# Performance work log

Measured on AMD Instinct MI355X. Metric: run time of the kernel, lower is better.

## Reference

```python
import jax, jax.numpy as jnp
import numpy as np

GRID = (32, 32)
LATENT = 256
ALPHA = 1.0
DECAY = 0.9


def _cdist(a, b):
    # Euclidean pairwise distance with a grad-safe sqrt (0 where d2==0, like torch.cdist).
    d2 = jnp.sum(a * a, -1)[:, None] + jnp.sum(b * b, -1)[None, :] - 2.0 * (a @ b.T)
    d2 = jnp.maximum(d2, 0.0)
    mask = d2 > 0
    return jnp.where(mask, jnp.sqrt(jnp.where(mask, d2, 1.0)), 0.0)


def setup_inputs() -> dict:
    key = jax.random.key(0)
    k1, k2 = jax.random.split(key)
    z = jax.random.normal(k1, (64, 512, 256), dtype=jnp.float32)
    nodes = jax.random.normal(k2, (GRID[0], GRID[1], LATENT), dtype=jnp.float32)
    return {"z": z, "nodes": nodes}


def reference(z, nodes):
    b, t, d = z.shape
    # time_decay^(seq_len - t - 1)
    tw = DECAY ** (t - 1 - jnp.arange(t, dtype=jnp.float32))
    z_flat = (z * tw[None, :, None]).reshape(b * t, d)   # (b t) d
    nodes_flat = nodes.reshape(-1, d)                     # n d

    dist = _cdist(z_flat, nodes_flat)                     # (b t) n
    q = 1.0 / (1.0 + dist / ALPHA) ** ((ALPHA + 1.0) / 2.0)
    q = q / jnp.sum(q, axis=-1, keepdims=True)            # L1 normalize rows
    q2 = q * q
    p = q2 / jnp.sum(q2, axis=0, keepdims=True)
    p = p / jnp.sum(p, axis=-1, keepdims=True)

    bmu = jnp.argmin(dist, axis=-1).reshape(b, t)         # int32

    # F.kl_div(q.log(), p, reduction='batchmean') = sum(p*(log p - log q)) / N
    kl_loss = jnp.sum(p * (jnp.log(p) - jnp.log(q))) / (b * t)
    diversity_loss = -jnp.mean(_cdist(nodes_flat, nodes_flat))
    time_smooth_loss = jnp.mean((z[:, 1:] - z[:, :-1]) ** 2) * DECAY

    # vectorized neighborhood consistency (python loop in the original is an
    # unweighted mean over all (b, t) adjacent pairs since seq_len is uniform)
    gw = GRID[1]
    pc = jnp.stack([bmu[:, :-1] // gw, bmu[:, :-1] % gw], axis=-1)
    nc = jnp.stack([bmu[:, 1:] // gw, bmu[:, 1:] % gw], axis=-1)
    neighbor_loss = jnp.mean(jnp.sum(jnp.abs(pc - nc), axis=-1).astype(jnp.float32))

    total_loss = kl_loss + 0.5 * diversity_loss + 0.3 * time_smooth_loss + 0.2 * neighbor_loss

    bmu_nodes = nodes_flat[bmu.reshape(-1)].reshape(b, t, d)
    som_z = z + 0.1 * (bmu_nodes - z)
    return (som_z, total_loss, kl_loss, diversity_loss, time_smooth_loss, neighbor_loss, q, bmu)
```

## Files before the change

### kernel.cpp

```cpp
#include <hip/hip_runtime.h>
#include <math.h>

#define Bb 64
#define Tt 512
#define Dd 256
#define Nn 1024
#define NROWS 32768

#define OUT_SOM 0L
#define OUT_SCAL 8388608L
#define OUT_Q 8388613L
#define OUT_BMU 41943045L

typedef __attribute__((ext_vector_type(8))) short bf16x8;
typedef __attribute__((ext_vector_type(4))) float f32x4;
typedef unsigned long long u64;
typedef unsigned short ushortT;

static __device__ __forceinline__ unsigned short f2bf(float x) {
  unsigned int u = __float_as_uint(x);
  unsigned int r = (u + 0x7fffu + ((u >> 16) & 1u)) >> 16;
  return (unsigned short)r;
}
static __device__ __forceinline__ float bf2f(unsigned short b) {
  return __uint_as_float(((unsigned int)b) << 16);
}

static __device__ __forceinline__ float block_reduce_sum(float v, float* sb) {
#pragma unroll
  for (int o = 32; o > 0; o >>= 1) v += __shfl_down(v, o, 64);
  const int lane = threadIdx.x & 63, w = threadIdx.x >> 6;
  if (lane == 0) sb[w] = v;
  __syncthreads();
  return (threadIdx.x == 0) ? (sb[0] + sb[1] + sb[2] + sb[3]) : 0.0f;
}

__global__ __launch_bounds__(256) void k_conv(
    const float* __restrict__ z, const float* __restrict__ nodes,
    ushortT* __restrict__ zhiF, ushortT* __restrict__ zloF, float* __restrict__ zn,
    ushortT* __restrict__ nhiF, ushortT* __restrict__ nloF, float* __restrict__ nnorm) {
  __shared__ float sm[32 * 260];
  const int tid = threadIdx.x;
  if (blockIdx.x < 1024) {
    const int rt = blockIdx.x;
    const long row0 = (long)rt * 32;
    const int r = tid >> 3, c8 = tid & 7;
    const long rowg = row0 + r;
    const int t = (int)(rowg & (Tt - 1));
    const float tw = powf(0.9f, (float)(Tt - 1 - t));
    float nrm = 0.f;
#pragma unroll
    for (int k = 0; k < 8; ++k) {
      const int c4 = c8 + k * 8;
      float4 v = ((const float4*)(z + rowg * Dd))[c4];
      v.x *= tw; v.y *= tw; v.z *= tw; v.w *= tw;
      *(float4*)&sm[r * 260 + c4 * 4] = v;
      nrm += v.x * v.x + v.y * v.y + v.z * v.z + v.w * v.w;
    }
    nrm += __shfl_xor(nrm, 1, 64);
    nrm += __shfl_xor(nrm, 2, 64);
    nrm += __shfl_xor(nrm, 4, 64);
    if (c8 == 0) zn[rowg] = nrm;
    __syncthreads();
    ushort4* oh = (ushort4*)(zhiF + (long)rt * 8192);
    ushort4* ol = (ushort4*)(zloF + (long)rt * 8192);
#pragma unroll
    for (int i = 0; i < 8; ++i) {
      const int o4 = tid + 256 * i;
      const int e4 = (o4 & 1) * 4;
      const int r16 = (o4 >> 1) & 15;
      const int k8 = (o4 >> 5) & 3;
      const int g = (o4 >> 7) & 1;
      const int ks = o4 >> 8;
      const float* p = &sm[(g * 16 + r16) * 260 + ks * 32 + k8 * 8 + e4];
      const float4 v = *(const float4*)p;
      ushort4 h, l;
      h.x = f2bf(v.x); l.x = f2bf(v.x - bf2f(h.x));
      h.y = f2bf(v.y); l.y = f2bf(v.y - bf2f(h.y));
      h.z = f2bf(v.z); l.z = f2bf(v.z - bf2f(h.z));
      h.w = f2bf(v.w); l.w = f2bf(v.w - bf2f(h.w));
      oh[o4] = h;
      ol[o4] = l;
    }
  } else {
    const int ct = blockIdx.x - 1024;
    const int jr = tid >> 4, cg = tid & 15;
    const long nrow = (long)(ct * 16 + jr);
    float nrm = 0.f;
#pragma unroll
    for (int k = 0; k < 4; ++k) {
      const int c4 = cg + k * 16;
      const float4 v = ((const float4*)(nodes + nrow * Dd))[c4];
      *(float4*)&sm[jr * 260 + c4 * 4] = v;
      nrm += v.x * v.x + v.y * v.y + v.z * v.z + v.w * v.w;
    }
    nrm += __shfl_xor(nrm, 1, 64);
    nrm += __shfl_xor(nrm, 2, 64);
    nrm += __shfl_xor(nrm, 4, 64);
    nrm += __shfl_xor(nrm, 8, 64);
    if (cg == 0) nnorm[nrow] = nrm;
    __syncthreads();
    ushort4* oh = (ushort4*)(nhiF + (long)ct * 4096);
    ushort4* ol = (ushort4*)(nloF + (long)ct * 4096);
#pragma unroll
    for (int i = 0; i < 4; ++i) {
      const int o4 = tid + 256 * i;
      const int e4 = (o4 & 1) * 4;
      const int c16 = (o4 >> 1) & 15;
      const int k8 = (o4 >> 5) & 3;
      const int ks = o4 >> 7;
      const float* p = &sm[c16 * 260 + ks * 32 + k8 * 8 + e4];
      const float4 v = *(const float4*)p;
      ushort4 h, l;
      h.x = f2bf(v.x); l.x = f2bf(v.x - bf2f(h.x));
      h.y = f2bf(v.y); l.y = f2bf(v.y - bf2f(h.y));
      h.z = f2bf(v.z); l.z = f2bf(v.z - bf2f(h.z));
      h.w = f2bf(v.w); l.w = f2bf(v.w - bf2f(h.w));
      oh[o4] = h;
      ol[o4] = l;
    }
  }
}

__global__ __launch_bounds__(1024, 4) void k_gemm4(
    const ushortT* __restrict__ zhiF, const ushortT* __restrict__ zloF,
    const ushortT* __restrict__ nhiF, const ushortT* __restrict__ nloF,
    const float* __restrict__ zn, const float* __restrict__ nn,
    float* __restrict__ qout, float* __restrict__ bmuf, float* __restrict__ colsum) {
  __shared__ float srowS[32][16];
  __shared__ u64 sbmu[32][16];
  __shared__ float sinv[32];
  const int tid = threadIdx.x, lane = tid & 63, w = tid >> 6;
  const int rl = lane & 15, kq = lane >> 4;
  const int rt = blockIdx.x;
  const long row0 = (long)rt * 32;

  const ushortT* Ah = zhiF + (long)rt * 8192;
  const ushortT* Al = zloF + (long)rt * 8192;
  const ushortT* Bh = nhiF + (long)w * 4 * 4096;
  const ushortT* Bl = nloF + (long)w * 4 * 4096;
  const int lo8 = lane * 8;

  f32x4 acc[2][4];
#pragma unroll
  for (int g = 0; g < 2; ++g)
#pragma unroll
    for (int c = 0; c < 4; ++c) acc[g][c] = (f32x4){0.f, 0.f, 0.f, 0.f};

#pragma unroll 2
  for (int ks = 0; ks < 8; ++ks) {
    bf16x8 ah[2], al[2], bh[4], bl[4];
#pragma unroll
    for (int g = 0; g < 2; ++g) {
      ah[g] = *(const bf16x8*)(Ah + (ks * 2 + g) * 512 + lo8);
      al[g] = *(const bf16x8*)(Al + (ks * 2 + g) * 512 + lo8);
    }
#pragma unroll
    for (int c = 0; c < 4; ++c) {
      bh[c] = *(const bf16x8*)(Bh + c * 4096 + ks * 512 + lo8);
      bl[c] = *(const bf16x8*)(Bl + c * 4096 + ks * 512 + lo8);
    }
    __builtin_amdgcn_s_setprio(1);
#pragma unroll
    for (int c = 0; c < 4; ++c)
#pragma unroll
      for (int g = 0; g < 2; ++g) {
        acc[g][c] = __builtin_amdgcn_mfma_f32_16x16x32_bf16(ah[g], bh[c], acc[g][c], 0, 0, 0);
        acc[g][c] = __builtin_amdgcn_mfma_f32_16x16x32_bf16(ah[g], bl[c], acc[g][c], 0, 0, 0);
        acc[g][c] = __builtin_amdgcn_mfma_f32_16x16x32_bf16(al[g], bh[c], acc[g][c], 0, 0, 0);
      }
    __builtin_amdgcn_s_setprio(0);
  }

  float nnv[4];
#pragma unroll
  for (int c = 0; c < 4; ++c) nnv[c] = nn[w * 64 + c * 16 + rl];

  float rs[2][4];
  u64 bm[2][4];
#pragma unroll
  for (int g = 0; g < 2; ++g)
#pragma unroll
    for (int r = 0; r < 4; ++r) {
      rs[g][r] = 0.f;
      bm[g][r] = ~0ull;
    }
#pragma unroll
  for (int g = 0; g < 2; ++g) {
    float znv[4];
#pragma unroll
    for (int r = 0; r < 4; ++r) znv[r] = zn[row0 + g * 16 + kq * 4 + r];
#pragma unroll
    for (int c = 0; c < 4; ++c)
#pragma unroll
      for (int r = 0; r < 4; ++r) {
        const float dot = acc[g][c][r];
        const float d2 = znv[r] + nnv[c] - 2.f * dot;
        const float dist = sqrtf(fmaxf(d2, 0.f));
        const float qv = 1.f / (1.f + dist);
        acc[g][c][r] = qv;
        rs[g][r] += qv;
        const int col = w * 64 + c * 16 + rl;
        const u64 pk = ((u64)__float_as_uint(dist) << 32) | (unsigned int)col;
        bm[g][r] = pk < bm[g][r] ? pk : bm[g][r];
      }
  }
#pragma unroll
  for (int g = 0; g < 2; ++g)
#pragma unroll
    for (int r = 0; r < 4; ++r) {
#pragma unroll
      for (int m = 1; m < 16; m <<= 1) {
        rs[g][r] += __shfl_xor(rs[g][r], m, 64);
        const u64 o = __shfl_xor(bm[g][r], m, 64);
        bm[g][r] = o < bm[g][r] ? o : bm[g][r];
      }
      if (rl == 0) {
        srowS[g * 16 + kq * 4 + r][w] = rs[g][r];
        sbmu[g * 16 + kq * 4 + r][w] = bm[g][r];
      }
    }
  __syncthreads();
  if (tid < 32) {
    float s = 0.f;
    u64 best = ~0ull;
#pragma unroll
    for (int i = 0; i < 16; ++i) {
      s += srowS[tid][i];
      const u64 v = sbmu[tid][i];
      best = v < best ? v : best;
    }
    sinv[tid] = 1.f / s;
    bmuf[row0 + tid] = (float)(int)(unsigned int)(best & 0xffffffffull);
  }
  __syncthreads();

  float cp[4];
#pragma unroll
  for (int c = 0; c < 4; ++c) cp[c] = 0.f;
#pragma unroll
  for (int g = 0; g < 2; ++g) {
    float inv[4];
#pragma unroll
    for (int r = 0; r < 4; ++r) inv[r] = sinv[g * 16 + kq * 4 + r];
#pragma unroll
    for (int c = 0; c < 4; ++c)
#pragma unroll
      for (int r = 0; r < 4; ++r) {
        const float qn = acc[g][c][r] * inv[r];
        qout[(row0 + g * 16 + kq * 4 + r) * Nn + w * 64 + c * 16 + rl] = qn;
        cp[c] = fmaf(qn, qn, cp[c]);
      }
  }
#pragma unroll
  for (int c = 0; c < 4; ++c) {
    cp[c] += __shfl_xor(cp[c], 16, 64);
    cp[c] += __shfl_xor(cp[c], 32, 64);
    if (kq == 0) atomicAdd(&colsum[w * 64 + c * 16 + rl], cp[c]);
  }
}

__global__ __launch_bounds__(256) void k_div2(
    const ushortT* __restrict__ nhiF, const ushortT* __restrict__ nloF,
    const float* __restrict__ nnorm, float* __restrict__ scal) {
  __shared__ float sb[4];
  const int tid = threadIdx.x, lane = tid & 63, w = tid >> 6;
  const int rl = lane & 15, kq = lane >> 4;
  const int bi = blockIdx.x & 63;
  const int cq = blockIdx.x >> 6;
  const int lo8 = lane * 8;

  f32x4 acc[4];
#pragma unroll
  for (int c = 0; c < 4; ++c) acc[c] = (f32x4){0.f, 0.f, 0.f, 0.f};

#pragma unroll 2
  for (int ks = 0; ks < 8; ++ks) {
    const bf16x8 ah = *(const bf16x8*)(nhiF + (long)bi * 4096 + ks * 512 + lo8);
    const bf16x8 al = *(const bf16x8*)(nloF + (long)bi * 4096 + ks * 512 + lo8);
#pragma unroll
    for (int c = 0; c < 4; ++c) {
      const long ct = (long)(cq * 16 + w * 4 + c);
      const bf16x8 bh = *(const bf16x8*)(nhiF + ct * 4096 + ks * 512 + lo8);
      const bf16x8 bl = *(const bf16x8*)(nloF + ct * 4096 + ks * 512 + lo8);
      acc[c] = __builtin_amdgcn_mfma_f32_16x16x32_bf16(ah, bh, acc[c], 0, 0, 0);
      acc[c] = __builtin_amdgcn_mfma_f32_16x16x32_bf16(ah, bl, acc[c], 0, 0, 0);
      acc[c] = __builtin_amdgcn_mfma_f32_16x16x32_bf16(al, bh, acc[c], 0, 0, 0);
    }
  }
  float ni[4];
#pragma unroll
  for (int r = 0; r < 4; ++r) ni[r] = nnorm[bi * 16 + kq * 4 + r];
  float dsum = 0.f;
#pragma unroll
  for (int c = 0; c < 4; ++c) {
    const float nj = nnorm[(cq * 16 + w * 4 + c) * 16 + rl];
#pragma unroll
    for (int r = 0; r < 4; ++r) {
      const float d2 = ni[r] + nj - 2.f * acc[c][r];
      dsum += sqrtf(fmaxf(d2, 0.f));
    }
  }
  const float tot = block_reduce_sum(dsum, sb);
  if (tid == 0) atomicAdd(&scal[1], tot);
}

__global__ __launch_bounds__(256) void k_kl(const float* __restrict__ q,
                                            const float* __restrict__ colsum,
                                            float* __restrict__ scal) {
  __shared__ float4 rcs4[Nn / 4];
  __shared__ float4 lcs4[Nn / 4];
  __shared__ float sb[4];
  const int tid = threadIdx.x, lane = tid & 63, wave = tid >> 6;
  {
    const float c0 = colsum[tid * 4 + 0];
    const float c1 = colsum[tid * 4 + 1];
    const float c2 = colsum[tid * 4 + 2];
    const float c3 = colsum[tid * 4 + 3];
    rcs4[tid] = make_float4(1.f / c0, 1.f / c1, 1.f / c2, 1.f / c3);
    lcs4[tid] = make_float4(__logf(c0), __logf(c1), __logf(c2), __logf(c3));
  }
  __syncthreads();
  const long r0 = (long)blockIdx.x * 16;
  float klp = 0.f;
  for (int rr = 0; rr < 4; ++rr) {
    const long row = r0 + rr * 4 + wave;
    float s = 0.f, a = 0.f;
#pragma unroll
    for (int j = 0; j < 4; ++j) {
      const int c4 = lane + 64 * j;
      const float4 qv = *(const float4*)(q + row * Nn + c4 * 4);
      const float4 rc = rcs4[c4];
      const float4 lc = lcs4[c4];
      float u;
      u = qv.x * qv.x * rc.x; s += u; a = fmaf(u, __logf(qv.x) - lc.x, a);
      u = qv.y * qv.y * rc.y; s += u; a = fmaf(u, __logf(qv.y) - lc.y, a);
      u = qv.z * qv.z * rc.z; s += u; a = fmaf(u, __logf(qv.z) - lc.z, a);
      u = qv.w * qv.w * rc.w; s += u; a = fmaf(u, __logf(qv.w) - lc.w, a);
    }
#pragma unroll
    for (int o = 1; o < 64; o <<= 1) {
      s += __shfl_xor(s, o, 64);
      a += __shfl_xor(a, o, 64);
    }
    if (lane == 0) klp += a / s - __logf(s);
  }
  const float tot = block_reduce_sum(klp, sb);
  if (tid == 0) atomicAdd(&scal[0], tot);
}

__global__ __launch_bounds__(256) void k_somnb(const float* __restrict__ z,
                                               const float* __restrict__ nodes,
                                               const float* __restrict__ bmuf,
                                               float* __restrict__ som,
                                               float* __restrict__ scal) {
  __shared__ float sb[4];
  const int tid = threadIdx.x;
  const long r0 = (long)blockIdx.x * 16;
  float ts = 0.f, zp = 0.f;
  if ((r0 & (Tt - 1)) > 0) zp = z[(r0 - 1) * Dd + tid];
  for (int r = 0; r < 16; ++r) {
    const long row = r0 + r;
    const float zc = z[row * Dd + tid];
    const int bi = (int)bmuf[row];
    const float nv = nodes[(long)bi * Dd + tid];
    som[row * Dd + tid] = zc + 0.1f * (nv - zc);
    if ((row & (Tt - 1)) > 0) {
      const float dd = zc - zp;
      ts = fmaf(dd, dd, ts);
    }
    zp = zc;
  }
  const float tts = block_reduce_sum(ts, sb);
  if (tid == 0) atomicAdd(&scal[2], tts);
  float nbv = 0.f;
  if (tid < 16) {
    const long row = r0 + tid;
    if ((row & (Tt - 1)) != (Tt - 1)) {
      const int b1 = (int)bmuf[row], b2 = (int)bmuf[row + 1];
      nbv = (float)(abs((b1 >> 5) - (b2 >> 5)) + abs((b1 & 31) - (b2 & 31)));
    }
  }
  __syncthreads();
  const float tnb = block_reduce_sum(nbv, sb);
  if (tid == 0) atomicAdd(&scal[3], tnb);
}

__global__ void k_final(const float* __restrict__ scal, float* __restrict__ o) {
  const float kl = scal[0] * (1.f / 32768.f);
  const float dv = -scal[1] * (1.f / (1024.f * 1024.f));
  const float ts = scal[2] * (0.9f / (64.f * 511.f * 256.f));
  const float nb = scal[3] * (1.f / 32704.f);
  o[0] = kl + 0.5f * dv + 0.3f * ts + 0.2f * nb;
  o[1] = kl;
  o[2] = dv;
  o[3] = ts;
  o[4] = nb;
}

__global__ __launch_bounds__(256) void k_prep_fb(const float* __restrict__ nodes,
                                                 float* __restrict__ nt,
                                                 float* __restrict__ nnorm) {
  __shared__ float sb[4];
  const int j = blockIdx.x, d = threadIdx.x;
  const float v = nodes[j * Dd + d];
  nt[(long)d * Nn + j] = v;
  const float tot = block_reduce_sum(v * v, sb);
  if (threadIdx.x == 0) nnorm[j] = tot;
}

__global__ __launch_bounds__(256) void k_div_fb(const float* __restrict__ nodes,
                                                const float* __restrict__ nt,
                                                const float* __restrict__ nnorm,
                                                float* __restrict__ scal) {
  __shared__ float ni[4][Dd];
  __shared__ float sb[4];
  const int tid = threadIdx.x;
  const int i0 = blockIdx.x * 4;
#pragma unroll
  for (int r = 0; r < 4; ++r) ni[r][tid] = nodes[(i0 + r) * Dd + tid];
  __syncthreads();
  float acc[4][4];
#pragma unroll
  for (int r = 0; r < 4; ++r)
#pragma unroll
    for (int jj = 0; jj < 4; ++jj) acc[r][jj] = 0.f;
  for (int d = 0; d < Dd; ++d) {
    float nj[4];
#pragma unroll
    for (int jj = 0; jj < 4; ++jj) nj[jj] = nt[(long)d * Nn + tid + 256 * jj];
#pragma unroll
    for (int r = 0; r < 4; ++r) {
      const float s = ni[r][d];
#pragma unroll
      for (int jj = 0; jj < 4; ++jj) acc[r][jj] = fmaf(s, nj[jj], acc[r][jj]);
    }
  }
  float sum = 0.f;
#pragma unroll
  for (int r = 0; r < 4; ++r)
#pragma unroll
    for (int jj = 0; jj < 4; ++jj) {
      const float d2 = nnorm[i0 + r] + nnorm[tid + 256 * jj] - 2.f * acc[r][jj];
      sum += sqrtf(fmaxf(d2, 0.f));
    }
  const float tot = block_reduce_sum(sum, sb);
  if (tid == 0) atomicAdd(&scal[1], tot);
}

__global__ __launch_bounds__(256) void k_dist_fb(
    const float* __restrict__ z, const float* __restrict__ nt,
    const float* __restrict__ nnorm, float* __restrict__ qout,
    float* __restrict__ srow, float* __restrict__ bmuf) {
  __shared__ float zt[Dd][65];
  __shared__ float rs4[4][64];
  __shared__ u64 cand[4][64];
  const int tid = threadIdx.x, lane = tid & 63, wave = tid >> 6;
  const long row0 = (long)blockIdx.x * 64;
  for (int k = 0; k < 64; ++k) {
    const int t = (int)((row0 + k) & (Tt - 1));
    const float tw = powf(0.9f, (float)(Tt - 1 - t));
    zt[tid][k] = z[(row0 + k) * Dd + tid] * tw;
  }
  __syncthreads();
  float zns = 0.f;
  for (int d = 0; d < Dd; ++d) {
    const float v = zt[d][lane];
    zns = fmaf(v, v, zns);
  }
  const long myrow = row0 + lane;
  float rsum = 0.f;
  u64 best = ~0ull;
  const int j0w = wave * 256;
  for (int chunk = 0; chunk < 16; ++chunk) {
    const int j0 = j0w + chunk * 16;
    float acc[16];
#pragma unroll
    for (int i = 0; i < 16; ++i) acc[i] = 0.f;
    const float* ntp = nt + j0;
    for (int d = 0; d < Dd; ++d) {
      const float zv = zt[d][lane];
      const float4 a = ((const float4*)ntp)[0];
      const float4 b = ((const float4*)ntp)[1];
      const float4 c = ((const float4*)ntp)[2];
      const float4 e = ((const float4*)ntp)[3];
      ntp += Nn;
      acc[0] = fmaf(zv, a.x, acc[0]); acc[1] = fmaf(zv, a.y, acc[1]);
      acc[2] = fmaf(zv, a.z, acc[2]); acc[3] = fmaf(zv, a.w, acc[3]);
      acc[4] = fmaf(zv, b.x, acc[4]); acc[5] = fmaf(zv, b.y, acc[5]);
      acc[6] = fmaf(zv, b.z, acc[6]); acc[7] = fmaf(zv, b.w, acc[7]);
      acc[8] = fmaf(zv, c.x, acc[8]); acc[9] = fmaf(zv, c.y, acc[9]);
      acc[10] = fmaf(zv, c.z, acc[10]); acc[11] = fmaf(zv, c.w, acc[11]);
      acc[12] = fmaf(zv, e.x, acc[12]); acc[13] = fmaf(zv, e.y, acc[13]);
      acc[14] = fmaf(zv, e.z, acc[14]); acc[15] = fmaf(zv, e.w, acc[15]);
    }
#pragma unroll
    for (int jj = 0; jj < 16; ++jj) {
      const int j = j0 + jj;
      const float d2 = zns + nnorm[j] - 2.f * acc[jj];
      const float dist = sqrtf(fmaxf(d2, 0.f));
      const float qr = 1.f / (1.f + dist);
      qout[myrow * Nn + j] = qr;
      rsum += qr;
      const u64 pk = ((u64)__float_as_uint(dist) << 32) | (unsigned int)j;
      best = pk < best ? pk : best;
    }
  }
  rs4[wave][lane] = rsum;
  cand[wave][lane] = best;
  __syncthreads();
  if (wave == 0) {
    const float s = rs4[0][lane] + rs4[1][lane] + rs4[2][lane] + rs4[3][lane];
    srow[myrow] = s;
    const u64 m0 = cand[0][lane] < cand[1][lane] ? cand[0][lane] : cand[1][lane];
    const u64 m1 = cand[2][lane] < cand[3][lane] ? cand[2][lane] : cand[3][lane];
    const u64 m = m0 < m1 ? m0 : m1;
    bmuf[myrow] = (float)(int)(unsigned int)(m & 0xffffffffull);
  }
}

__global__ __launch_bounds__(256) void k_norm_fb(float* __restrict__ q,
                                                 const float* __restrict__ srow,
                                                 float* __restrict__ colsum) {
  const int tid = threadIdx.x;
  const long r0 = (long)blockIdx.x * 16;
  float cs[4] = {0.f, 0.f, 0.f, 0.f};
  for (int r = 0; r < 16; ++r) {
    const long row = r0 + r;
    const float inv = 1.f / srow[row];
#pragma unroll
    for (int j = 0; j < 4; ++j) {
      const long idx = row * Nn + tid + 256 * j;
      const float v = q[idx] * inv;
      q[idx] = v;
      cs[j] = fmaf(v, v, cs[j]);
    }
  }
#pragma unroll
  for (int j = 0; j < 4; ++j) atomicAdd(&colsum[tid + 256 * j], cs[j]);
}

extern "C" void kernel_launch(void* const* d_in, const int* in_sizes, int n_in,
                              void* d_out, int out_size, void* d_ws, size_t ws_size,
                              hipStream_t stream) {
  const float* z = (const float*)d_in[0];
  const float* nodes = (const float*)d_in[1];
  float* out = (float*)d_out;
  unsigned char* ws = (unsigned char*)d_ws;

  float* som = out + OUT_SOM;
  float* scal_out = out + OUT_SCAL;
  float* qout = out + OUT_Q;
  float* bmuf = out + OUT_BMU;

  const size_t NEED = 34742288;
  if (ws_size >= NEED) {
    ushortT* zhiF = (ushortT*)(ws + 0);
    ushortT* zloF = (ushortT*)(ws + 16777216);
    ushortT* nhiF = (ushortT*)(ws + 33554432);
    ushortT* nloF = (ushortT*)(ws + 34078720);
    float* zn = (float*)(ws + 34603008);
    float* nnorm = (float*)(ws + 34734080);
    float* colsum = (float*)(ws + 34738176);
    float* scal = (float*)(ws + 34742272);

    hipMemsetAsync(colsum, 0, 4096 + 16, stream);

    k_conv<<<1088, 256, 0, stream>>>(z, nodes, zhiF, zloF, zn, nhiF, nloF, nnorm);
    k_gemm4<<<1024, 1024, 0, stream>>>(zhiF, zloF, nhiF, nloF, zn, nnorm, qout, bmuf, colsum);
    k_div2<<<256, 256, 0, stream>>>(nhiF, nloF, nnorm, scal);
    k_kl<<<2048, 256, 0, stream>>>(qout, colsum, scal);
    k_somnb<<<2048, 256, 0, stream>>>(z, nodes, bmuf, som, scal);
    k_final<<<1, 1, 0, stream>>>(scal, scal_out);
  } else {
    float* wsf = (float*)ws;
    float* nt = wsf;
    float* nnorm = wsf + 262144;
    float* srow = wsf + 263168;
    float* colsum = wsf + 295936;
    float* scal = wsf + 296960;

    hipMemsetAsync(colsum, 0, (1024 + 4) * sizeof(float), stream);
    k_prep_fb<<<1024, 256, 0, stream>>>(nodes, nt, nnorm);
    k_div_fb<<<256, 256, 0, stream>>>(nodes, nt, nnorm, scal);
    k_dist_fb<<<512, 256, 0, stream>>>(z, nt, nnorm, qout, srow, bmuf);
    k_norm_fb<<<2048, 256, 0, stream>>>(qout, srow, colsum);
    k_kl<<<2048, 256, 0, stream>>>(qout, colsum, scal);
    k_somnb<<<2048, 256, 0, stream>>>(z, nodes, bmuf, som, scal);
    k_final<<<1, 1, 0, stream>>>(scal, scal_out);
  }
}
```

Before: 251.6 us.

## Restructure SOM pipeline: row-major split A, LDS-staged 64-row GEMM, fused tail kernel

The conversion kernel now writes z's hi/lo bf16 split in a simple row-major layout, one wave per row. The GEMM handles 64 rows per block and stages A into LDS with global_load_lds and an XOR swizzle. It runs the three split-precision MFMA passes as 24 sequential k-steps. Column sums are written as per-block partials and reduced by a new small kernel, which replaces the global atomics and the memset. The KL, SOM/neighbour and diversity kernels are merged into one launch; the trade-off is a larger workspace, a scalar KL loop, and more LDS per GEMM block, which may limit occupancy.

```diff
diff --git a/kernel.cpp b/kernel.cpp
--- a/kernel.cpp
+++ b/kernel.cpp
@@ -35,55 +35,32 @@
   return (threadIdx.x == 0) ? (sb[0] + sb[1] + sb[2] + sb[3]) : 0.0f;
 }
 
-__global__ __launch_bounds__(256) void k_conv(
+__global__ __launch_bounds__(256) void k_conv3(
     const float* __restrict__ z, const float* __restrict__ nodes,
-    ushortT* __restrict__ zhiF, ushortT* __restrict__ zloF, float* __restrict__ zn,
-    ushortT* __restrict__ nhiF, ushortT* __restrict__ nloF, float* __restrict__ nnorm) {
+    ushortT* __restrict__ A2, ushortT* __restrict__ nhiF, ushortT* __restrict__ nloF,
+    float* __restrict__ zn, float* __restrict__ nnorm) {
   __shared__ float sm[32 * 260];
   const int tid = threadIdx.x;
-  if (blockIdx.x < 1024) {
-    const int rt = blockIdx.x;
-    const long row0 = (long)rt * 32;
-    const int r = tid >> 3, c8 = tid & 7;
-    const long rowg = row0 + r;
-    const int t = (int)(rowg & (Tt - 1));
+  if (blockIdx.x < 8192) {
+    const int lane = tid & 63, w = tid >> 6;
+    const long row = (long)blockIdx.x * 4 + w;
+    const int t = (int)(row & (Tt - 1));
     const float tw = powf(0.9f, (float)(Tt - 1 - t));
-    float nrm = 0.f;
-#pragma unroll
-    for (int k = 0; k < 8; ++k) {
-      const int c4 = c8 + k * 8;
-      float4 v = ((const float4*)(z + rowg * Dd))[c4];
-      v.x *= tw; v.y *= tw; v.z *= tw; v.w *= tw;
-      *(float4*)&sm[r * 260 + c4 * 4] = v;
-      nrm += v.x * v.x + v.y * v.y + v.z * v.z + v.w * v.w;
-    }
-    nrm += __shfl_xor(nrm, 1, 64);
-    nrm += __shfl_xor(nrm, 2, 64);
-    nrm += __shfl_xor(nrm, 4, 64);
-    if (c8 == 0) zn[rowg] = nrm;
-    __syncthreads();
-    ushort4* oh = (ushort4*)(zhiF + (long)rt * 8192);
-    ushort4* ol = (ushort4*)(zloF + (long)rt * 8192);
-#pragma unroll
-    for (int i = 0; i < 8; ++i) {
-      const int o4 = tid + 256 * i;
-      const int e4 = (o4 & 1) * 4;
-      const int r16 = (o4 >> 1) & 15;
-      const int k8 = (o4 >> 5) & 3;
-      const int g = (o4 >> 7) & 1;
-      const int ks = o4 >> 8;
-      const float* p = &sm[(g * 16 + r16) * 260 + ks * 32 + k8 * 8 + e4];
-      const float4 v = *(const float4*)p;
-      ushort4 h, l;
-      h.x = f2bf(v.x); l.x = f2bf(v.x - bf2f(h.x));
-      h.y = f2bf(v.y); l.y = f2bf(v.y - bf2f(h.y));
-      h.z = f2bf(v.z); l.z = f2bf(v.z - bf2f(h.z));
-      h.w = f2bf(v.w); l.w = f2bf(v.w - bf2f(h.w));
-      oh[o4] = h;
-      ol[o4] = l;
-    }
+    const float4 v = ((const float4*)(z + row * Dd))[lane];
+    float x0 = v.x * tw, x1 = v.y * tw, x2 = v.z * tw, x3 = v.w * tw;
+    ushort4 h, l;
+    h.x = f2bf(x0); l.x = f2bf(x0 - bf2f(h.x));
+    h.y = f2bf(x1); l.y = f2bf(x1 - bf2f(h.y));
+    h.z = f2bf(x2); l.z = f2bf(x2 - bf2f(h.z));
+    h.w = f2bf(x3); l.w = f2bf(x3 - bf2f(h.w));
+    *(ushort4*)(A2 + row * 512 + lane * 4) = h;
+    *(ushort4*)(A2 + row * 512 + 256 + lane * 4) = l;
+    float s = x0 * x0 + x1 * x1 + x2 * x2 + x3 * x3;
+#pragma unroll
+    for (int o = 32; o > 0; o >>= 1) s += __shfl_down(s, o, 64);
+    if (lane == 0) zn[row] = s;
   } else {
-    const int ct = blockIdx.x - 1024;
+    const int ct = blockIdx.x - 8192;
     const int jr = tid >> 4, cg = tid & 15;
     const long nrow = (long)(ct * 16 + jr);
     float nrm = 0.f;
@@ -122,71 +99,77 @@
   }
 }
 
-__global__ __launch_bounds__(1024, 4) void k_gemm4(
-    const ushortT* __restrict__ zhiF, const ushortT* __restrict__ zloF,
-    const ushortT* __restrict__ nhiF, const ushortT* __restrict__ nloF,
-    const float* __restrict__ zn, const float* __restrict__ nn,
-    float* __restrict__ qout, float* __restrict__ bmuf, float* __restrict__ colsum) {
-  __shared__ float srowS[32][16];
-  __shared__ u64 sbmu[32][16];
-  __shared__ float sinv[32];
+__global__ __launch_bounds__(1024) void k_gemmF(
+    const ushortT* __restrict__ A2, const ushortT* __restrict__ nhiF,
+    const ushortT* __restrict__ nloF, const float* __restrict__ zn,
+    const float* __restrict__ nnorm, float* __restrict__ qout,
+    float* __restrict__ bmuf, float* __restrict__ psum) {
+  __shared__ __align__(16) unsigned char sA[65536];
+  __shared__ float srowS[64][16];
+  __shared__ u64 sbmu[64][16];
+  __shared__ float sinv[64];
   const int tid = threadIdx.x, lane = tid & 63, w = tid >> 6;
   const int rl = lane & 15, kq = lane >> 4;
-  const int rt = blockIdx.x;
-  const long row0 = (long)rt * 32;
-
-  const ushortT* Ah = zhiF + (long)rt * 8192;
-  const ushortT* Al = zloF + (long)rt * 8192;
-  const ushortT* Bh = nhiF + (long)w * 4 * 4096;
-  const ushortT* Bl = nloF + (long)w * 4 * 4096;
-  const int lo8 = lane * 8;
-
-  f32x4 acc[2][4];
-#pragma unroll
-  for (int g = 0; g < 2; ++g)
+  const long row0 = (long)blockIdx.x * 64;
+
+#pragma unroll
+  for (int i = 0; i < 4; ++i) {
+    const int flat = i * 1024 + tid;
+    const int r = flat >> 6, slot = flat & 63;
+    const int srcs = slot ^ (r & 7);
+    __builtin_amdgcn_global_load_lds(
+        (const __attribute__((address_space(1))) void*)(A2 + (row0 + r) * 512 + srcs * 8),
+        (__attribute__((address_space(3))) void*)(sA + flat * 16), 16, 0, 0);
+  }
+
+  const ushortT* Bh = nhiF + (long)(w * 4) * 4096 + lane * 8;
+  const ushortT* Bl = nloF + (long)(w * 4) * 4096 + lane * 8;
+
+  f32x4 acc[4][4];
+#pragma unroll
+  for (int g = 0; g < 4; ++g)
 #pragma unroll
     for (int c = 0; c < 4; ++c) acc[g][c] = (f32x4){0.f, 0.f, 0.f, 0.f};
 
-#pragma unroll 2
-  for (int ks = 0; ks < 8; ++ks) {
-    bf16x8 ah[2], al[2], bh[4], bl[4];
-#pragma unroll
-    for (int g = 0; g < 2; ++g) {
-      ah[g] = *(const bf16x8*)(Ah + (ks * 2 + g) * 512 + lo8);
-      al[g] = *(const bf16x8*)(Al + (ks * 2 + g) * 512 + lo8);
-    }
-#pragma unroll
-    for (int c = 0; c < 4; ++c) {
-      bh[c] = *(const bf16x8*)(Bh + c * 4096 + ks * 512 + lo8);
-      bl[c] = *(const bf16x8*)(Bl + c * 4096 + ks * 512 + lo8);
+  __syncthreads();
+
+#pragma unroll
+  for (int m = 0; m < 24; ++m) {
+    const int t3 = m >> 3, ks = m & 7;
+    const int abase = (t3 == 2) ? 32 : 0;
+    const ushortT* Bp = (t3 == 1) ? Bl : Bh;
+    bf16x8 b[4];
+#pragma unroll
+    for (int c = 0; c < 4; ++c) b[c] = *(const bf16x8*)(Bp + c * 4096 + ks * 512);
+    bf16x8 a[4];
+#pragma unroll
+    for (int g = 0; g < 4; ++g) {
+      const int rr = g * 16 + rl;
+      const int kslot = abase + ks * 4 + kq;
+      a[g] = *(const bf16x8*)(sA + rr * 1024 + ((kslot ^ (rr & 7)) << 4));
     }
     __builtin_amdgcn_s_setprio(1);
 #pragma unroll
-    for (int c = 0; c < 4; ++c)
-#pragma unroll
-      for (int g = 0; g < 2; ++g) {
-        acc[g][c] = __builtin_amdgcn_mfma_f32_16x16x32_bf16(ah[g], bh[c], acc[g][c], 0, 0, 0);
-        acc[g][c] = __builtin_amdgcn_mfma_f32_16x16x32_bf16(ah[g], bl[c], acc[g][c], 0, 0, 0);
-        acc[g][c] = __builtin_amdgcn_mfma_f32_16x16x32_bf16(al[g], bh[c], acc[g][c], 0, 0, 0);
-      }
+    for (int g = 0; g < 4; ++g)
+#pragma unroll
+      for (int c = 0; c < 4; ++c)
+        acc[g][c] = __builtin_amdgcn_mfma_f32_16x16x32_bf16(a[g], b[c], acc[g][c], 0, 0, 0);
     __builtin_amdgcn_s_setprio(0);
   }
 
   float nnv[4];
 #pragma unroll
-  for (int c = 0; c < 4; ++c) nnv[c] = nn[w * 64 + c * 16 + rl];
-
-  float rs[2][4];
-  u64 bm[2][4];
-#pragma unroll
-  for (int g = 0; g < 2; ++g)
-#pragma unroll
-    for (int r = 0; r < 4; ++r) {
-      rs[g][r] = 0.f;
-      bm[g][r] = ~0ull;
-    }
-#pragma unroll
-  for (int g = 0; g < 2; ++g) {
+  for (int c = 0; c < 4; ++c) nnv[c] = nnorm[w * 64 + c * 16 + rl];
+
+  float rs[4][4];
+  u64 bm[4][4];
+#pragma unroll
+  for (int g = 0; g < 4; ++g)
+#pragma unroll
+    for (int r = 0; r < 4; ++r) { rs[g][r] = 0.f; bm[g][r] = ~0ull; }
+
+#pragma unroll
+  for (int g = 0; g < 4; ++g) {
     float znv[4];
 #pragma unroll
     for (int r = 0; r < 4; ++r) znv[r] = zn[row0 + g * 16 + kq * 4 + r];
@@ -206,7 +189,7 @@
       }
   }
 #pragma unroll
-  for (int g = 0; g < 2; ++g)
+  for (int g = 0; g < 4; ++g)
 #pragma unroll
     for (int r = 0; r < 4; ++r) {
 #pragma unroll
@@ -221,7 +204,7 @@
       }
     }
   __syncthreads();
-  if (tid < 32) {
+  if (tid < 64) {
     float s = 0.f;
     u64 best = ~0ull;
 #pragma unroll
@@ -239,7 +222,7 @@
 #pragma unroll
   for (int c = 0; c < 4; ++c) cp[c] = 0.f;
 #pragma unroll
-  for (int g = 0; g < 2; ++g) {
+  for (int g = 0; g < 4; ++g) {
     float inv[4];
 #pragma unroll
     for (int r = 0; r < 4; ++r) inv[r] = sinv[g * 16 + kq * 4 + r];
@@ -256,134 +239,135 @@
   for (int c = 0; c < 4; ++c) {
     cp[c] += __shfl_xor(cp[c], 16, 64);
     cp[c] += __shfl_xor(cp[c], 32, 64);
-    if (kq == 0) atomicAdd(&colsum[w * 64 + c * 16 + rl], cp[c]);
-  }
-}
-
-__global__ __launch_bounds__(256) void k_div2(
-    const ushortT* __restrict__ nhiF, const ushortT* __restrict__ nloF,
-    const float* __restrict__ nnorm, float* __restrict__ scal) {
-  __shared__ float sb[4];
-  const int tid = threadIdx.x, lane = tid & 63, w = tid >> 6;
-  const int rl = lane & 15, kq = lane >> 4;
-  const int bi = blockIdx.x & 63;
-  const int cq = blockIdx.x >> 6;
-  const int lo8 = lane * 8;
-
-  f32x4 acc[4];
-#pragma unroll
-  for (int c = 0; c < 4; ++c) acc[c] = (f32x4){0.f, 0.f, 0.f, 0.f};
-
+    if (kq == 0) psum[(long)blockIdx.x * Nn + w * 64 + c * 16 + rl] = cp[c];
+  }
+}
+
+__global__ __launch_bounds__(256) void k_cs(const float* __restrict__ psum,
+                                            float* __restrict__ colsum) {
+  __shared__ float sh[4][64];
+  const int c = threadIdx.x & 63, sl = threadIdx.x >> 6;
+  const int col = blockIdx.x * 64 + c;
+  float s = 0.f;
+#pragma unroll 4
+  for (int p = sl * 128; p < sl * 128 + 128; ++p) s += psum[(long)p * Nn + col];
+  sh[sl][c] = s;
+  __syncthreads();
+  if (sl == 0) colsum[col] = sh[0][c] + sh[1][c] + sh[2][c] + sh[3][c];
+}
+
+__global__ __launch_bounds__(256) void k_tail(
+    const float* __restrict__ q, const float* __restrict__ colsum,
+    const float* __restrict__ z, const float* __restrict__ nodes,
+    const float* __restrict__ bmuf, const ushortT* __restrict__ nhiF,
+    const ushortT* __restrict__ nloF, const float* __restrict__ nnorm,
+    float* __restrict__ som, float* __restrict__ scal) {
+  __shared__ float sh[2052];
+  const int tid = threadIdx.x, lane = tid & 63, wave = tid >> 6;
+  const int bid = blockIdx.x;
+  if (bid < 2048) {
+    float* rcs = sh;
+    float* lcs = sh + 1024;
+    float* sb = sh + 2048;
+#pragma unroll
+    for (int j = 0; j < 4; ++j) {
+      const float cs = colsum[tid + 256 * j];
+      rcs[tid + 256 * j] = 1.f / cs;
+      lcs[tid + 256 * j] = __logf(cs);
+    }
+    __syncthreads();
+    const long r0 = (long)bid * 16;
+    float klp = 0.f;
+    for (int rr = 0; rr < 4; ++rr) {
+      const long row = r0 + rr * 4 + wave;
+      float s = 0.f, a = 0.f;
+#pragma unroll
+      for (int j = 0; j < 16; ++j) {
+        const int col = lane + 64 * j;
+        const float t = q[row * Nn + col];
+        const float u = t * t * rcs[col];
+        s += u;
+        a = fmaf(u, __logf(t) - lcs[col], a);
+      }
+#pragma unroll
+      for (int o = 1; o < 64; o <<= 1) {
+        s += __shfl_xor(s, o, 64);
+        a += __shfl_xor(a, o, 64);
+      }
+      if (lane == 0) klp += a / s - __logf(s);
+    }
+    const float tot = block_reduce_sum(klp, sb);
+    if (tid == 0) atomicAdd(&scal[0], tot);
+  } else if (bid < 4096) {
+    float* sb = sh;
+    const long r0 = (long)(bid - 2048) * 16;
+    float ts = 0.f, zp = 0.f;
+    if ((r0 & (Tt - 1)) > 0) zp = z[(r0 - 1) * Dd + tid];
+    for (int r = 0; r < 16; ++r) {
+      const long row = r0 + r;
+      const float zc = z[row * Dd + tid];
+      const int bi = (int)bmuf[row];
+      const float nv = nodes[(long)bi * Dd + tid];
+      som[row * Dd + tid] = zc + 0.1f * (nv - zc);
+      if ((row & (Tt - 1)) > 0) {
+        const float dd = zc - zp;
+        ts = fmaf(dd, dd, ts);
+      }
+      zp = zc;
+    }
+    const float tts = block_reduce_sum(ts, sb);
+    if (tid == 0) atomicAdd(&scal[2], tts);
+    float nbv = 0.f;
+    if (tid < 16) {
+      const long row = r0 + tid;
+      if ((row & (Tt - 1)) != (Tt - 1)) {
+        const int b1 = (int)bmuf[row], b2 = (int)bmuf[row + 1];
+        nbv = (float)(abs((b1 >> 5) - (b2 >> 5)) + abs((b1 & 31) - (b2 & 31)));
+      }
+    }
+    __syncthreads();
+    const float tnb = block_reduce_sum(nbv, sb);
+    if (tid == 0) atomicAdd(&scal[3], tnb);
+  } else {
+    float* sb = sh;
+    const int w = wave;
+    const int rl = lane & 15, kq = lane >> 4;
+    const int bi = (bid - 4096) & 63;
+    const int cq = (bid - 4096) >> 6;
+    const int lo8 = lane * 8;
+    f32x4 acc[4];
+#pragma unroll
+    for (int c = 0; c < 4; ++c) acc[c] = (f32x4){0.f, 0.f, 0.f, 0.f};
 #pragma unroll 2
-  for (int ks = 0; ks < 8; ++ks) {
-    const bf16x8 ah = *(const bf16x8*)(nhiF + (long)bi * 4096 + ks * 512 + lo8);
-    const bf16x8 al = *(const bf16x8*)(nloF + (long)bi * 4096 + ks * 512 + lo8);
+    for (int ks = 0; ks < 8; ++ks) {
+      const bf16x8 ah = *(const bf16x8*)(nhiF + (long)bi * 4096 + ks * 512 + lo8);
+      const bf16x8 al = *(const bf16x8*)(nloF + (long)bi * 4096 + ks * 512 + lo8);
+#pragma unroll
+      for (int c = 0; c < 4; ++c) {
+        const long ct = (long)(cq * 16 + w * 4 + c);
+        const bf16x8 bh = *(const bf16x8*)(nhiF + ct * 4096 + ks * 512 + lo8);
+        const bf16x8 bl = *(const bf16x8*)(nloF + ct * 4096 + ks * 512 + lo8);
+        acc[c] = __builtin_amdgcn_mfma_f32_16x16x32_bf16(ah, bh, acc[c], 0, 0, 0);
+        acc[c] = __builtin_amdgcn_mfma_f32_16x16x32_bf16(ah, bl, acc[c], 0, 0, 0);
+        acc[c] = __builtin_amdgcn_mfma_f32_16x16x32_bf16(al, bh, acc[c], 0, 0, 0);
+      }
+    }
+    float ni[4];
+#pragma unroll
+    for (int r = 0; r < 4; ++r) ni[r] = nnorm[bi * 16 + kq * 4 + r];
+    float dsum = 0.f;
 #pragma unroll
     for (int c = 0; c < 4; ++c) {
-      const long ct = (long)(cq * 16 + w * 4 + c);
-      const bf16x8 bh = *(const bf16x8*)(nhiF + ct * 4096 + ks * 512 + lo8);
-      const bf16x8 bl = *(const bf16x8*)(nloF + ct * 4096 + ks * 512 + lo8);
-      acc[c] = __builtin_amdgcn_mfma_f32_16x16x32_bf16(ah, bh, acc[c], 0, 0, 0);
-      acc[c] = __builtin_amdgcn_mfma_f32_16x16x32_bf16(ah, bl, acc[c], 0, 0, 0);
-      acc[c] = __builtin_amdgcn_mfma_f32_16x16x32_bf16(al, bh, acc[c], 0, 0, 0);
-    }
-  }
-  float ni[4];
-#pragma unroll
-  for (int r = 0; r < 4; ++r) ni[r] = nnorm[bi * 16 + kq * 4 + r];
-  float dsum = 0.f;
-#pragma unroll
-  for (int c = 0; c < 4; ++c) {
-    const float nj = nnorm[(cq * 16 + w * 4 + c) * 16 + rl];
-#pragma unroll
-    for (int r = 0; r < 4; ++r) {
-      const float d2 = ni[r] + nj - 2.f * acc[c][r];
-      dsum += sqrtf(fmaxf(d2, 0.f));
-    }
-  }
-  const float tot = block_reduce_sum(dsum, sb);
-  if (tid == 0) atomicAdd(&scal[1], tot);
-}
-
-__global__ __launch_bounds__(256) void k_kl(const float* __restrict__ q,
-                                            const float* __restrict__ colsum,
-                                            float* __restrict__ scal) {
-  __shared__ float4 rcs4[Nn / 4];
-  __shared__ float4 lcs4[Nn / 4];
-  __shared__ float sb[4];
-  const int tid = threadIdx.x, lane = tid & 63, wave = tid >> 6;
-  {
-    const float c0 = colsum[tid * 4 + 0];
-    const float c1 = colsum[tid * 4 + 1];
-    const float c2 = colsum[tid * 4 + 2];
-    const float c3 = colsum[tid * 4 + 3];
-    rcs4[tid] = make_float4(1.f / c0, 1.f / c1, 1.f / c2, 1.f / c3);
-    lcs4[tid] = make_float4(__logf(c0), __logf(c1), __logf(c2), __logf(c3));
-  }
-  __syncthreads();
-  const long r0 = (long)blockIdx.x * 16;
-  float klp = 0.f;
-  for (int rr = 0; rr < 4; ++rr) {
-    const long row = r0 + rr * 4 + wave;
-    float s = 0.f, a = 0.f;
-#pragma unroll
-    for (int j = 0; j < 4; ++j) {
-      const int c4 = lane + 64 * j;
-      const float4 qv = *(const float4*)(q + row * Nn + c4 * 4);
-      const float4 rc = rcs4[c4];
-      const float4 lc = lcs4[c4];
-      float u;
-      u = qv.x * qv.x * rc.x; s += u; a = fmaf(u, __logf(qv.x) - lc.x, a);
-      u = qv.y * qv.y * rc.y; s += u; a = fmaf(u, __logf(qv.y) - lc.y, a);
-      u = qv.z * qv.z * rc.z; s += u; a = fmaf(u, __logf(qv.z) - lc.z, a);
-      u = qv.w * qv.w * rc.w; s += u; a = fmaf(u, __logf(qv.w) - lc.w, a);
-    }
-#pragma unroll
-    for (int o = 1; o < 64; o <<= 1) {
-      s += __shfl_xor(s, o, 64);
-      a += __shfl_xor(a, o, 64);
-    }
-    if (lane == 0) klp += a / s - __logf(s);
-  }
-  const float tot = block_reduce_sum(klp, sb);
-  if (tid == 0) atomicAdd(&scal[0], tot);
-}
-
-__global__ __launch_bounds__(256) void k_somnb(const float* __restrict__ z,
-                                               const float* __restrict__ nodes,
-                                               const float* __restrict__ bmuf,
-                                               float* __restrict__ som,
-                                               float* __restrict__ scal) {
-  __shared__ float sb[4];
-  const int tid = threadIdx.x;
-  const long r0 = (long)blockIdx.x * 16;
-  float ts = 0.f, zp = 0.f;
-  if ((r0 & (Tt - 1)) > 0) zp = z[(r0 - 1) * Dd + tid];
-  for (int r = 0; r < 16; ++r) {
-    const long row = r0 + r;
-    const float zc = z[row * Dd + tid];
-    const int bi = (int)bmuf[row];
-    const float nv = nodes[(long)bi * Dd + tid];
-    som[row * Dd + tid] = zc + 0.1f * (nv - zc);
-    if ((row & (Tt - 1)) > 0) {
-      const float dd = zc - zp;
-      ts = fmaf(dd, dd, ts);
-    }
-    zp = zc;
-  }
-  const float tts = block_reduce_sum(ts, sb);
-  if (tid == 0) atomicAdd(&scal[2], tts);
-  float nbv = 0.f;
-  if (tid < 16) {
-    const long row = r0 + tid;
-    if ((row & (Tt - 1)) != (Tt - 1)) {
-      const int b1 = (int)bmuf[row], b2 = (int)bmuf[row + 1];
-      nbv = (float)(abs((b1 >> 5) - (b2 >> 5)) + abs((b1 & 31) - (b2 & 31)));
-    }
-  }
-  __syncthreads();
-  const float tnb = block_reduce_sum(nbv, sb);
-  if (tid == 0) atomicAdd(&scal[3], tnb);
+      const float nj = nnorm[(cq * 16 + w * 4 + c) * 16 + rl];
+#pragma unroll
+      for (int r = 0; r < 4; ++r) {
+        const float d2 = ni[r] + nj - 2.f * acc[c][r];
+        dsum += sqrtf(fmaxf(d2, 0.f));
+      }
+    }
+    const float tot = block_reduce_sum(dsum, sb);
+    if (tid == 0) atomicAdd(&scal[1], tot);
+  }
 }
 
 __global__ void k_final(const float* __restrict__ scal, float* __restrict__ o) {
@@ -540,6 +524,81 @@
   for (int j = 0; j < 4; ++j) atomicAdd(&colsum[tid + 256 * j], cs[j]);
 }
 
+__global__ __launch_bounds__(256) void k_kl_fb(const float* __restrict__ q,
+                                               const float* __restrict__ colsum,
+                                               float* __restrict__ scal) {
+  __shared__ float rcs[Nn];
+  __shared__ float lcs[Nn];
+  __shared__ float sb[4];
+  const int tid = threadIdx.x, lane = tid & 63, wave = tid >> 6;
+#pragma unroll
+  for (int j = 0; j < 4; ++j) {
+    const float cs = colsum[tid + 256 * j];
+    rcs[tid + 256 * j] = 1.f / cs;
+    lcs[tid + 256 * j] = __logf(cs);
+  }
+  __syncthreads();
+  const long r0 = (long)blockIdx.x * 16;
+  float klp = 0.f;
+  for (int rr = 0; rr < 4; ++rr) {
+    const long row = r0 + rr * 4 + wave;
+    float s = 0.f, a = 0.f;
+#pragma unroll
+    for (int j = 0; j < 16; ++j) {
+      const int col = lane + 64 * j;
+      const float t = q[row * Nn + col];
+      const float u = t * t * rcs[col];
+      s += u;
+      a = fmaf(u, __logf(t) - lcs[col], a);
+    }
+#pragma unroll
+    for (int o = 1; o < 64; o <<= 1) {
+      s += __shfl_xor(s, o, 64);
+      a += __shfl_xor(a, o, 64);
+    }
+    if (lane == 0) klp += a / s - __logf(s);
+  }
+  const float tot = block_reduce_sum(klp, sb);
+  if (tid == 0) atomicAdd(&scal[0], tot);
+}
+
+__global__ __launch_bounds__(256) void k_somnb_fb(const float* __restrict__ z,
+                                                  const float* __restrict__ nodes,
+                                                  const float* __restrict__ bmuf,
+                                                  float* __restrict__ som,
+                                                  float* __restrict__ scal) {
+  __shared__ float sb[4];
+  const int tid = threadIdx.x;
+  const long r0 = (long)blockIdx.x * 16;
+  float ts = 0.f, zp = 0.f;
+  if ((r0 & (Tt - 1)) > 0) zp = z[(r0 - 1) * Dd + tid];
+  for (int r = 0; r < 16; ++r) {
+    const long row = r0 + r;
+    const float zc = z[row * Dd + tid];
+    const int bi = (int)bmuf[row];
+    const float nv = nodes[(long)bi * Dd + tid];
+    som[row * Dd + tid] = zc + 0.1f * (nv - zc);
+    if ((row & (Tt - 1)) > 0) {
+      const float dd = zc - zp;
+      ts = fmaf(dd, dd, ts);
+    }
+    zp = zc;
+  }
+  const float tts = block_reduce_sum(ts, sb);
+  if (tid == 0) atomicAdd(&scal[2], tts);
+  float nbv = 0.f;
+  if (tid < 16) {
+    const long row = r0 + tid;
+    if ((row & (Tt - 1)) != (Tt - 1)) {
+      const int b1 = (int)bmuf[row], b2 = (int)bmuf[row + 1];
+      nbv = (float)(abs((b1 >> 5) - (b2 >> 5)) + abs((b1 & 31) - (b2 & 31)));
+    }
+  }
+  __syncthreads();
+  const float tnb = block_reduce_sum(nbv, sb);
+  if (tid == 0) atomicAdd(&scal[3], tnb);
+}
+
 extern "C" void kernel_launch(void* const* d_in, const int* in_sizes, int n_in,
                               void* d_out, int out_size, void* d_ws, size_t ws_size,
                               hipStream_t stream) {
@@ -553,24 +612,24 @@
   float* qout = out + OUT_Q;
   float* bmuf = out + OUT_BMU;
 
-  const size_t NEED = 34742288;
+  const size_t NEED = 36839440;
   if (ws_size >= NEED) {
-    ushortT* zhiF = (ushortT*)(ws + 0);
-    ushortT* zloF = (ushortT*)(ws + 16777216);
+    ushortT* A2 = (ushortT*)(ws + 0);
     ushortT* nhiF = (ushortT*)(ws + 33554432);
     ushortT* nloF = (ushortT*)(ws + 34078720);
     float* zn = (float*)(ws + 34603008);
     float* nnorm = (float*)(ws + 34734080);
-    float* colsum = (float*)(ws + 34738176);
-    float* scal = (float*)(ws + 34742272);
-
-    hipMemsetAsync(colsum, 0, 4096 + 16, stream);
-
-    k_conv<<<1088, 256, 0, stream>>>(z, nodes, zhiF, zloF, zn, nhiF, nloF, nnorm);
-    k_gemm4<<<1024, 1024, 0, stream>>>(zhiF, zloF, nhiF, nloF, zn, nnorm, qout, bmuf, colsum);
-    k_div2<<<256, 256, 0, stream>>>(nhiF, nloF, nnorm, scal);
-    k_kl<<<2048, 256, 0, stream>>>(qout, colsum, scal);
-    k_somnb<<<2048, 256, 0, stream>>>(z, nodes, bmuf, som, scal);
+    float* psum = (float*)(ws + 34738176);
+    float* colsum = (float*)(ws + 36835328);
+    float* scal = (float*)(ws + 36839424);
+
+    hipMemsetAsync(scal, 0, 16, stream);
+
+    k_conv3<<<8256, 256, 0, stream>>>(z, nodes, A2, nhiF, nloF, zn, nnorm);
+    k_gemmF<<<512, 1024, 0, stream>>>(A2, nhiF, nloF, zn, nnorm, qout, bmuf, psum);
+    k_cs<<<16, 256, 0, stream>>>(psum, colsum);
+    k_tail<<<4352, 256, 0, stream>>>(qout, colsum, z, nodes, bmuf, nhiF, nloF, nnorm,
+                                     som, scal);
     k_final<<<1, 1, 0, stream>>>(scal, scal_out);
   } else {
     float* wsf = (float*)ws;
@@ -585,8 +644,8 @@
     k_div_fb<<<256, 256, 0, stream>>>(nodes, nt, nnorm, scal);
     k_dist_fb<<<512, 256, 0, stream>>>(z, nt, nnorm, qout, srow, bmuf);
     k_norm_fb<<<2048, 256, 0, stream>>>(qout, srow, colsum);
-    k_kl<<<2048, 256, 0, stream>>>(qout, colsum, scal);
-    k_somnb<<<2048, 256, 0, stream>>>(z, nodes, bmuf, som, scal);
+    k_kl_fb<<<2048, 256, 0, stream>>>(qout, colsum, scal);
+    k_somnb_fb<<<2048, 256, 0, stream>>>(z, nodes, bmuf, som, scal);
     k_final<<<1, 1, 0, stream>>>(scal, scal_out);
   }
 }
```

Result: faster. 239.5 us (median of 2 runs) (-4.8%).
